# Kernel tuning notes

Hardware: AMD Instinct MI355X
Metric: run time of the kernel (lower is better)

Reference implementation:

```python
import jax, jax.numpy as jnp
import numpy as np

COST_CLASS = 1.0


def _lsa(cost):
    """linear_sum_assignment clone (Jonker-Volgenant shortest augmenting path),
    matching scipy.optimize.linear_sum_assignment semantics for rectangular inputs."""
    cost = np.asarray(cost, dtype=np.float64)
    transposed = cost.shape[0] > cost.shape[1]
    if transposed:
        cost = cost.T
    nr, nc = cost.shape
    u = np.zeros(nr)
    v = np.zeros(nc)
    path = np.full(nc, -1, dtype=np.int64)
    col4row = np.full(nr, -1, dtype=np.int64)
    row4col = np.full(nc, -1, dtype=np.int64)
    for cur in range(nr):
        i = cur
        SR = np.zeros(nr, dtype=bool)
        SC = np.zeros(nc, dtype=bool)
        d = np.full(nc, np.inf)
        minVal = 0.0
        sink = -1
        while sink == -1:
            SR[i] = True
            rem = ~SC
            r = minVal + cost[i, rem] - u[i] - v[rem]
            dr = d[rem]
            pr = path[rem]
            better = r < dr
            dr[better] = r[better]
            pr[better] = i
            d[rem] = dr
            path[rem] = pr
            remIdx = np.flatnonzero(rem)
            j = remIdx[np.argmin(d[remIdx])]
            minVal = d[j]
            SC[j] = True
            if row4col[j] == -1:
                sink = j
            else:
                i = row4col[j]
        # dual updates (scipy _lsap_body)
        u[cur] += minVal
        mask = SR.copy()
        mask[cur] = False
        u[mask] += minVal - d[col4row[mask]]
        v[SC] -= minVal - d[SC]
        # augment along shortest path
        j = sink
        while True:
            i = path[j]
            row4col[j] = i
            col4row[i], j = j, col4row[i]
            if i == cur:
                break
    if transposed:
        order = np.argsort(col4row)
        return col4row[order], order
    return np.arange(nr), col4row


def setup_inputs() -> dict:
    key = jax.random.key(0)
    k1, k2, k3 = jax.random.split(key, 3)
    bs, Q, T, NC = 32, 256, 128, 2048
    pred_logits = jax.random.normal(k1, (bs, Q, NC), dtype=jnp.float32)
    tgt_labels = jax.random.randint(k2, (bs, T), 0, NC)
    agent_mask = jax.random.randint(k3, (bs, Q), 0, 2).astype(bool)
    return {"pred_logits": pred_logits, "tgt_labels": tgt_labels,
            "agent_mask": agent_mask, "use_background": 0}


def reference(pred_logits, tgt_labels, agent_mask, use_background):
    bs, Q, _ = pred_logits.shape
    T = tgt_labels.shape[1]
    probs = jax.nn.softmax(pred_logits, axis=-1)  # [bs, Q, NC]
    if not use_background:
        probs = jnp.where(agent_mask[:, :, None], probs, 0.0)
    out_prob = probs.reshape(bs * Q, -1)
    tgt_ids = tgt_labels.reshape(-1)                  # concat of all batch labels
    C = COST_CLASS * (-out_prob[:, tgt_ids])          # [bs*Q, bs*T]
    C = C.reshape(bs, Q, bs * T)
    # per-batch Hungarian (same as scipy loop in the original; inherently serial per instance)
    Cn = np.asarray(C)
    rows = np.empty((bs, T), dtype=np.int64)
    cols = np.empty((bs, T), dtype=np.int64)
    for i in range(bs):
        r, c = _lsa(Cn[i, :, i * T:(i + 1) * T])      # [Q, T] block for batch i
        rows[i] = r
        cols[i] = c
    return C, jnp.asarray(rows), jnp.asarray(cols)
```

## Files before the change

kernel.cpp:

```cpp
#include <hip/hip_runtime.h>
#include <hip/hip_bf16.h>
#include <math.h>

#define BS 32
#define QN 256
#define TN 128
#define NCLS 2048
#define NTGT (BS * TN)

__global__ void detect_mask_layout(const unsigned char* __restrict__ m, int* flag) {
    __shared__ int found;
    if (threadIdx.x == 0) found = 0;
    __syncthreads();
    int local = 0;
    for (int i = threadIdx.x; i < BS * QN; i += blockDim.x) {
        if ((i & 3) != 0 && m[i] != 0) local = 1;
    }
    if (local) atomicOr(&found, 1);
    __syncthreads();
    if (threadIdx.x == 0) *flag = found;
}

__global__ __launch_bounds__(256) void compute_C_kernel(
    const float* __restrict__ logits, const int* __restrict__ labels,
    const unsigned char* __restrict__ mask_b, const int* __restrict__ use_bg,
    const int* __restrict__ layout_flag, float* __restrict__ C) {
    __shared__ float prob_sh[NCLS];
    __shared__ int lab_sh[NTGT];
    __shared__ float red[4];

    const int tid = threadIdx.x;
    const int bq = blockIdx.x;
    const float* row = logits + (size_t)bq * NCLS;

    for (int k = tid; k < NTGT; k += 256) lab_sh[k] = labels[k];

    float x[8];
    float m = -INFINITY;
#pragma unroll
    for (int k = 0; k < 8; k++) {
        x[k] = row[tid + k * 256];
        m = fmaxf(m, x[k]);
    }
#pragma unroll
    for (int off = 32; off >= 1; off >>= 1) m = fmaxf(m, __shfl_xor(m, off));
    if ((tid & 63) == 0) red[tid >> 6] = m;
    __syncthreads();
    m = fmaxf(fmaxf(red[0], red[1]), fmaxf(red[2], red[3]));
    __syncthreads();

    float e[8];
    float s = 0.f;
#pragma unroll
    for (int k = 0; k < 8; k++) {
        e[k] = expf(x[k] - m);
        s += e[k];
    }
#pragma unroll
    for (int off = 32; off >= 1; off >>= 1) s += __shfl_xor(s, off);
    if ((tid & 63) == 0) red[tid >> 6] = s;
    __syncthreads();
    s = ((red[0] + red[1]) + red[2]) + red[3];

#pragma unroll
    for (int k = 0; k < 8; k++) prob_sh[tid + k * 256] = e[k] / s;

    const int ub = *use_bg;
    int am;
    if (*layout_flag)
        am = mask_b[bq];
    else
        am = ((const int*)mask_b)[bq];
    const bool zero_row = (ub == 0) && (am == 0);
    __syncthreads();

    float* Crow = C + (size_t)bq * NTGT;
#pragma unroll
    for (int k = 0; k < 16; k++) {
        const int jj = tid + k * 256;
        Crow[jj] = zero_row ? 0.0f : -prob_sh[lab_sh[jj]];
    }
}

__global__ __launch_bounds__(256) void transpose_kernel(const float* __restrict__ C,
                                                        float* __restrict__ CT) {
    __shared__ float tile[TN][65];
    const int b = blockIdx.x;
    const int q0 = blockIdx.y * 64;
    const int tid = threadIdx.x;

    const float* src = C + (size_t)(b * QN + q0) * NTGT + b * TN;
#pragma unroll
    for (int it = 0; it < 32; it++) {
        const int idx = tid + it * 256;
        const int ql = idx >> 7;
        const int i = idx & 127;
        tile[i][ql] = src[(size_t)ql * NTGT + i];
    }
    __syncthreads();
    float* dst = CT + (size_t)b * TN * QN + q0;
#pragma unroll
    for (int it = 0; it < 32; it++) {
        const int idx = tid + it * 256;
        const int i = idx >> 6;
        const int ql = idx & 63;
        dst[(size_t)i * QN + ql] = tile[i][ql];
    }
}

template <int CTRL>
__device__ __forceinline__ double dpp_mov_f64(double x) {
    union { double d; int i[2]; } a, r;
    a.d = x;
    r.i[0] = __builtin_amdgcn_update_dpp(0, a.i[0], CTRL, 0xF, 0xF, true);
    r.i[1] = __builtin_amdgcn_update_dpp(0, a.i[1], CTRL, 0xF, 0xF, true);
    return r.d;
}
__device__ __forceinline__ double read_lane_f64(double x, int srclane) {
    union { double d; int i[2]; } a, r;
    a.d = x;
    r.i[0] = __builtin_amdgcn_readlane(a.i[0], srclane);
    r.i[1] = __builtin_amdgcn_readlane(a.i[1], srclane);
    return r.d;
}

#define QUAD_XOR1 0xB1
#define QUAD_XOR2 0x4E
#define ROW_ROR4  0x124
#define ROW_ROR8  0x128

__device__ __forceinline__ int first_tied(unsigned long long B0, unsigned long long B1,
                                          unsigned long long B2, unsigned long long B3) {
    int jmin = 0x7fffffff;
    if (B0) { const int c = ((__ffsll((long long)B0) - 1) << 2) + 0; jmin = c < jmin ? c : jmin; }
    if (B1) { const int c = ((__ffsll((long long)B1) - 1) << 2) + 1; jmin = c < jmin ? c : jmin; }
    if (B2) { const int c = ((__ffsll((long long)B2) - 1) << 2) + 2; jmin = c < jmin ? c : jmin; }
    if (B3) { const int c = ((__ffsll((long long)B3) - 1) << 2) + 3; jmin = c < jmin ? c : jmin; }
    return jmin;
}

__global__ __launch_bounds__(64) void lsa_kernel(const float* __restrict__ C,
                                                 const float* __restrict__ CT,
                                                 float* __restrict__ rows_out,
                                                 float* __restrict__ cols_out) {
    const int b = blockIdx.x;
    const int lane = threadIdx.x;
    const int j0 = lane * 4;

    __shared__ float cost_sh[TN * QN];
    __shared__ double u_sh[TN];
    __shared__ int col4row_sh[TN];

    if (CT) {
        const float4* src = (const float4*)(CT + (size_t)b * TN * QN);
        float4* dst = (float4*)cost_sh;
#pragma unroll 8
        for (int it = 0; it < TN * QN / 4 / 64; it++) {
            const int idx = it * 64 + lane;
            dst[idx] = src[idx];
        }
    } else {
        const float* cbsrc = C + (size_t)b * QN * NTGT + b * TN;
        for (int it = 0; it < 512; it++) {
            const int j = it >> 1;
            const int i = lane + 64 * (it & 1);
            cost_sh[i * QN + j] = cbsrc[(size_t)j * NTGT + i];
        }
    }
    u_sh[2 * lane] = 0.0;
    u_sh[2 * lane + 1] = 0.0;
    __syncthreads();

    double v0 = 0.0, v1 = 0.0, v2 = 0.0, v3 = 0.0;
    double u0 = 0.0, u1 = 0.0;
    int rc0 = -1, rc1 = -1, rc2 = -1, rc3 = -1;
    int cr0 = -1, cr1 = -1;

    for (int cur = 0; cur < TN; cur++) {
        double dv0 = INFINITY, dv1 = INFINITY, dv2 = INFINITY, dv3 = INFINITY;
        double duA = 0.0, duB = 0.0;
        int sc = 0, sr = 0;
        int p0 = 0, p1 = 0, p2 = 0, p3 = 0;
        if (lane == (cur >> 1)) sr = 1 << (cur & 1);

        int i = cur;
        double m_d = 0.0;
        unsigned long long B0 = 0, B1 = 0, B2 = 0, B3 = 0;
        int sink = 0;
        bool have_g = false;
        int jg = 0, krcg = 0;

        float4 cc = *(const float4*)(cost_sh + i * QN + j0);
        double ui = u_sh[i];
        float4 gcc = cc;
        double gui = ui;

        while (true) {
            const double ca0 = ((m_d + (double)cc.x) - ui) - v0;
            const double ca1 = ((m_d + (double)cc.y) - ui) - v1;
            const double ca2 = ((m_d + (double)cc.z) - ui) - v2;
            const double ca3 = ((m_d + (double)cc.w) - ui) - v3;
            const bool i0 = !(sc & 1) && (ca0 < dv0);
            const bool i1 = !(sc & 2) && (ca1 < dv1);
            const bool i2 = !(sc & 4) && (ca2 < dv2);
            const bool i3 = !(sc & 8) && (ca3 < dv3);
            const unsigned long long chk =
                __ballot(i0 && (ca0 <= m_d)) | __ballot(i1 && (ca1 <= m_d)) |
                __ballot(i2 && (ca2 <= m_d)) | __ballot(i3 && (ca3 <= m_d));
            if (i0) { dv0 = ca0; p0 = i; }
            if (i1) { dv1 = ca1; p1 = i; }
            if (i2) { dv2 = ca2; p2 = i; }
            if (i3) { dv3 = ca3; p3 = i; }

            if (chk == 0ull && have_g) {
                if (krcg < 0) { sink = jg; break; }
                const int gowner = jg >> 2;
                const int gslot = jg & 3;
                if (lane == gowner) sc |= 1 << gslot;
                if (lane == (krcg >> 1)) {
                    if (krcg & 1) { duB = m_d; sr |= 2; }
                    else { duA = m_d; sr |= 1; }
                }
                i = krcg;
                cc = gcc;
                ui = gui;
            } else {
                const double md0 = (sc & 1) ? INFINITY : dv0;
                const double md1 = (sc & 2) ? INFINITY : dv1;
                const double md2 = (sc & 4) ? INFINITY : dv2;
                const double md3 = (sc & 8) ? INFINITY : dv3;
                double lm = fmin(fmin(md0, md1), fmin(md2, md3));
                lm = fmin(lm, dpp_mov_f64<QUAD_XOR1>(lm));
                lm = fmin(lm, dpp_mov_f64<QUAD_XOR2>(lm));
                lm = fmin(lm, dpp_mov_f64<ROW_ROR4>(lm));
                lm = fmin(lm, dpp_mov_f64<ROW_ROR8>(lm));
                const double r0 = read_lane_f64(lm, 0);
                const double r1 = read_lane_f64(lm, 16);
                const double r2 = read_lane_f64(lm, 32);
                const double r3 = read_lane_f64(lm, 48);
                m_d = fmin(fmin(r0, r1), fmin(r2, r3));
                B0 = __ballot(!(sc & 1) && (dv0 == m_d));
                B1 = __ballot(!(sc & 2) && (dv1 == m_d));
                B2 = __ballot(!(sc & 4) && (dv2 == m_d));
                B3 = __ballot(!(sc & 8) && (dv3 == m_d));

                const int jmin = first_tied(B0, B1, B2, B3);
                const int owner = jmin >> 2;
                const int slot = jmin & 3;
                const unsigned long long bit = 1ull << owner;
                if (slot == 0) B0 &= ~bit;
                else if (slot == 1) B1 &= ~bit;
                else if (slot == 2) B2 &= ~bit;
                else B3 &= ~bit;
                const int rsel = (slot == 0) ? rc0 : (slot == 1) ? rc1 : (slot == 2) ? rc2 : rc3;
                const int krc = __builtin_amdgcn_readlane(rsel, owner);
                if (krc < 0) { sink = jmin; break; }
                if (lane == owner) sc |= 1 << slot;
                if (lane == (krc >> 1)) {
                    if (krc & 1) { duB = m_d; sr |= 2; }
                    else { duA = m_d; sr |= 1; }
                }
                i = krc;
                cc = *(const float4*)(cost_sh + i * QN + j0);
                ui = u_sh[i];
            }

            if ((B0 | B1 | B2 | B3) != 0ull) {
                jg = first_tied(B0, B1, B2, B3);
                const int go = jg >> 2;
                const int gs = jg & 3;
                const unsigned long long gbit = 1ull << go;
                if (gs == 0) B0 &= ~gbit;
                else if (gs == 1) B1 &= ~gbit;
                else if (gs == 2) B2 &= ~gbit;
                else B3 &= ~gbit;
                const int grsel = (gs == 0) ? rc0 : (gs == 1) ? rc1 : (gs == 2) ? rc2 : rc3;
                krcg = __builtin_amdgcn_readlane(grsel, go);
                const int rg = (krcg >= 0) ? krcg : 0;
                gcc = *(const float4*)(cost_sh + rg * QN + j0);
                gui = u_sh[rg];
                have_g = true;
            } else {
                have_g = false;
            }
        }

        if (sc & 1) v0 -= m_d - dv0;
        if (sc & 2) v1 -= m_d - dv1;
        if (sc & 4) v2 -= m_d - dv2;
        if (sc & 8) v3 -= m_d - dv3;
        if (sr & 1) u0 += (2 * lane == cur) ? m_d : (m_d - duA);
        if (sr & 2) u1 += (2 * lane + 1 == cur) ? m_d : (m_d - duB);
        u_sh[2 * lane] = u0;
        u_sh[2 * lane + 1] = u1;

        int j = sink;
        while (true) {
            const int aslot = j & 3;
            const int aowner = j >> 2;
            const int psel = (aslot == 0) ? p0 : (aslot == 1) ? p1 : (aslot == 2) ? p2 : p3;
            const int pi = __builtin_amdgcn_readlane(psel, aowner);
            if (lane == aowner) {
                if (aslot == 0) rc0 = pi;
                else if (aslot == 1) rc1 = pi;
                else if (aslot == 2) rc2 = pi;
                else rc3 = pi;
            }
            const int cowner = pi >> 1;
            const int cslot = pi & 1;
            const int csel = cslot ? cr1 : cr0;
            const int nj = __builtin_amdgcn_readlane(csel, cowner);
            if (lane == cowner) {
                if (cslot) cr1 = j;
                else cr0 = j;
            }
            j = nj;
            if (pi == cur) break;
        }
    }

    col4row_sh[2 * lane] = cr0;
    col4row_sh[2 * lane + 1] = cr1;
    __syncthreads();
#pragma unroll
    for (int t = 0; t < 2; t++) {
        const int ii = 2 * lane + t;
        const int myv = t ? cr1 : cr0;
        int rank = 0;
        for (int t2 = 0; t2 < TN; t2++) rank += (col4row_sh[t2] < myv) ? 1 : 0;
        rows_out[b * TN + rank] = (float)myv;
        cols_out[b * TN + rank] = (float)ii;
    }
}

extern "C" void kernel_launch(void* const* d_in, const int* in_sizes, int n_in,
                              void* d_out, int out_size, void* d_ws, size_t ws_size,
                              hipStream_t stream) {
    const float* logits = (const float*)d_in[0];
    const int* labels = (const int*)d_in[1];
    const unsigned char* mask_b = (const unsigned char*)d_in[2];
    const int* use_bg = (const int*)d_in[3];

    float* C = (float*)d_out;
    float* rows_out = C + (size_t)BS * QN * NTGT;
    float* cols_out = rows_out + BS * TN;

    int* flag = (int*)d_ws;
    const size_t ct_off = 4096;
    const size_t ct_bytes = (size_t)BS * TN * QN * sizeof(float);
    const bool useCT = ws_size >= ct_off + ct_bytes;
    float* CT = useCT ? (float*)((char*)d_ws + ct_off) : nullptr;

    detect_mask_layout<<<1, 256, 0, stream>>>(mask_b, flag);
    compute_C_kernel<<<BS * QN, 256, 0, stream>>>(logits, labels, mask_b, use_bg, flag, C);
    if (useCT) {
        dim3 tg(BS, QN / 64);
        transpose_kernel<<<tg, 256, 0, stream>>>(C, CT);
    }
    lsa_kernel<<<BS, 64, 0, stream>>>(C, CT, rows_out, cols_out);
}
```

Measured before the change: 1.256 ms.

## Fuse transpose into cost kernel, vectorize C stores, and double-buffer LSA row loads

The separate transpose kernel is removed. The cost kernel now writes the transposed per-batch diagonal block directly, and it stores C rows as float4 using vectorized label reads. In the Hungarian loop, the body is unrolled twice with ping-pong registers so that the cost row for the next guessed pivot is prefetched before the current relaxation. The four chk ballots are also merged into one. This cuts a kernel launch and a pass over C, and hides shared-memory latency on the serial augmenting path. The trade-offs are strided scattered CT writes and an unconditional speculative load on every iteration.

Result: slower. 1.308 ms (+4.2%).

```diff
diff --git a/kernel.cpp b/kernel.cpp
--- a/kernel.cpp
+++ b/kernel.cpp
@@ -24,13 +24,16 @@
 __global__ __launch_bounds__(256) void compute_C_kernel(
     const float* __restrict__ logits, const int* __restrict__ labels,
     const unsigned char* __restrict__ mask_b, const int* __restrict__ use_bg,
-    const int* __restrict__ layout_flag, float* __restrict__ C) {
+    const int* __restrict__ layout_flag, float* __restrict__ C,
+    float* __restrict__ CT) {
     __shared__ float prob_sh[NCLS];
     __shared__ int lab_sh[NTGT];
     __shared__ float red[4];
 
     const int tid = threadIdx.x;
     const int bq = blockIdx.x;
+    const int b = bq >> 8;
+    const int q = bq & 255;
     const float* row = logits + (size_t)bq * NCLS;
 
     for (int k = tid; k < NTGT; k += 256) lab_sh[k] = labels[k];
@@ -74,37 +77,26 @@
     const bool zero_row = (ub == 0) && (am == 0);
     __syncthreads();
 
-    float* Crow = C + (size_t)bq * NTGT;
-#pragma unroll
-    for (int k = 0; k < 16; k++) {
-        const int jj = tid + k * 256;
-        Crow[jj] = zero_row ? 0.0f : -prob_sh[lab_sh[jj]];
-    }
-}
-
-__global__ __launch_bounds__(256) void transpose_kernel(const float* __restrict__ C,
-                                                        float* __restrict__ CT) {
-    __shared__ float tile[TN][65];
-    const int b = blockIdx.x;
-    const int q0 = blockIdx.y * 64;
-    const int tid = threadIdx.x;
-
-    const float* src = C + (size_t)(b * QN + q0) * NTGT + b * TN;
-#pragma unroll
-    for (int it = 0; it < 32; it++) {
-        const int idx = tid + it * 256;
-        const int ql = idx >> 7;
-        const int i = idx & 127;
-        tile[i][ql] = src[(size_t)ql * NTGT + i];
-    }
-    __syncthreads();
-    float* dst = CT + (size_t)b * TN * QN + q0;
-#pragma unroll
-    for (int it = 0; it < 32; it++) {
-        const int idx = tid + it * 256;
-        const int i = idx >> 6;
-        const int ql = idx & 63;
-        dst[(size_t)i * QN + ql] = tile[i][ql];
+    float4* Crow4 = (float4*)(C + (size_t)bq * NTGT);
+#pragma unroll
+    for (int k = 0; k < 4; k++) {
+        const int idx4 = tid + k * 256;
+        const int4 lab4 = *(const int4*)&lab_sh[idx4 * 4];
+        float4 out;
+        if (zero_row) {
+            out = make_float4(0.f, 0.f, 0.f, 0.f);
+        } else {
+            out.x = -prob_sh[lab4.x];
+            out.y = -prob_sh[lab4.y];
+            out.z = -prob_sh[lab4.z];
+            out.w = -prob_sh[lab4.w];
+        }
+        Crow4[idx4] = out;
+    }
+
+    if (CT && tid < TN) {
+        const float val = zero_row ? 0.0f : -prob_sh[lab_sh[b * TN + tid]];
+        CT[((size_t)b * TN + tid) * QN + q] = val;
     }
 }
 
@@ -178,119 +170,135 @@
 
     for (int cur = 0; cur < TN; cur++) {
         double dv0 = INFINITY, dv1 = INFINITY, dv2 = INFINITY, dv3 = INFINITY;
-        double duA = 0.0, duB = 0.0;
+        double duR0 = 0.0, duR1 = 0.0;
         int sc = 0, sr = 0;
         int p0 = 0, p1 = 0, p2 = 0, p3 = 0;
         if (lane == (cur >> 1)) sr = 1 << (cur & 1);
 
-        int i = cur;
+        int irow = cur;
         double m_d = 0.0;
         unsigned long long B0 = 0, B1 = 0, B2 = 0, B3 = 0;
-        int sink = 0;
+        int sink = -1;
         bool have_g = false;
         int jg = 0, krcg = 0;
 
-        float4 cc = *(const float4*)(cost_sh + i * QN + j0);
-        double ui = u_sh[i];
-        float4 gcc = cc;
-        double gui = ui;
+        float4 ccA = *(const float4*)(cost_sh + irow * QN + j0);
+        double uiA = u_sh[irow];
+        float4 ccB;
+        double uiB;
+
+#define POP_BODY(CCX, UIX, CCY, UIY)                                           \
+        {                                                                      \
+                          \
+            const int rg_ = (have_g && krcg >= 0) ? krcg : 0;                  \
+            CCY = *(const float4*)(cost_sh + rg_ * QN + j0);                   \
+            UIY = u_sh[rg_];                                                   \
+                             \
+            const double ca0 = ((m_d + (double)CCX.x) - UIX) - v0;             \
+            const double ca1 = ((m_d + (double)CCX.y) - UIX) - v1;             \
+            const double ca2 = ((m_d + (double)CCX.z) - UIX) - v2;             \
+            const double ca3 = ((m_d + (double)CCX.w) - UIX) - v3;             \
+            const bool i0_ = !(sc & 1) && (ca0 < dv0);                         \
+            const bool i1_ = !(sc & 2) && (ca1 < dv1);                         \
+            const bool i2_ = !(sc & 4) && (ca2 < dv2);                         \
+            const bool i3_ = !(sc & 8) && (ca3 < dv3);                         \
+            const bool chkl_ = (i0_ && ca0 <= m_d) || (i1_ && ca1 <= m_d) ||   \
+                               (i2_ && ca2 <= m_d) || (i3_ && ca3 <= m_d);     \
+            const unsigned long long chk_ = __ballot(chkl_);                   \
+            if (i0_) { dv0 = ca0; p0 = irow; }                                 \
+            if (i1_) { dv1 = ca1; p1 = irow; }                                 \
+            if (i2_) { dv2 = ca2; p2 = irow; }                                 \
+            if (i3_) { dv3 = ca3; p3 = irow; }                                 \
+            if (chk_ == 0ull && have_g) {                                      \
+                                               \
+                if (krcg < 0) {                                                \
+                    sink = jg;                                                 \
+                } else {                                                       \
+                    const int ow_ = jg >> 2, sl_ = jg & 3;                     \
+                    if (lane == ow_) sc |= 1 << sl_;                           \
+                    if (lane == (krcg >> 1)) {                                 \
+                        if (krcg & 1) { duR1 = m_d; sr |= 2; }                 \
+                        else { duR0 = m_d; sr |= 1; }                          \
+                    }                                                          \
+                    irow = krcg;                                               \
+                }                                                              \
+            } else {                                                           \
+                                      \
+                const double md0_ = (sc & 1) ? INFINITY : dv0;                 \
+                const double md1_ = (sc & 2) ? INFINITY : dv1;                 \
+                const double md2_ = (sc & 4) ? INFINITY : dv2;                 \
+                const double md3_ = (sc & 8) ? INFINITY : dv3;                 \
+                double lm_ = fmin(fmin(md0_, md1_), fmin(md2_, md3_));         \
+                lm_ = fmin(lm_, dpp_mov_f64<QUAD_XOR1>(lm_));                  \
+                lm_ = fmin(lm_, dpp_mov_f64<QUAD_XOR2>(lm_));                  \
+                lm_ = fmin(lm_, dpp_mov_f64<ROW_ROR4>(lm_));                   \
+                lm_ = fmin(lm_, dpp_mov_f64<ROW_ROR8>(lm_));                   \
+                const double r0_ = read_lane_f64(lm_, 0);                      \
+                const double r1_ = read_lane_f64(lm_, 16);                     \
+                const double r2_ = read_lane_f64(lm_, 32);                     \
+                const double r3_ = read_lane_f64(lm_, 48);                     \
+                m_d = fmin(fmin(r0_, r1_), fmin(r2_, r3_));                    \
+                B0 = __ballot(!(sc & 1) && (dv0 == m_d));                      \
+                B1 = __ballot(!(sc & 2) && (dv1 == m_d));                      \
+                B2 = __ballot(!(sc & 4) && (dv2 == m_d));                      \
+                B3 = __ballot(!(sc & 8) && (dv3 == m_d));                      \
+                const int jmin_ = first_tied(B0, B1, B2, B3);                  \
+                const int ow_ = jmin_ >> 2, sl_ = jmin_ & 3;                   \
+                const unsigned long long bit_ = 1ull << ow_;                   \
+                if (sl_ == 0) B0 &= ~bit_;                                     \
+                else if (sl_ == 1) B1 &= ~bit_;                                \
+                else if (sl_ == 2) B2 &= ~bit_;                                \
+                else B3 &= ~bit_;                                              \
+                const int rsel_ = (sl_ == 0) ? rc0 : (sl_ == 1) ? rc1          \
+                                 : (sl_ == 2) ? rc2 : rc3;                     \
+                const int krc_ = __builtin_amdgcn_readlane(rsel_, ow_);        \
+                if (krc_ < 0) {                                                \
+                    sink = jmin_;                                              \
+                } else {                                                       \
+                    if (lane == ow_) sc |= 1 << sl_;                           \
+                    if (lane == (krc_ >> 1)) {                                 \
+                        if (krc_ & 1) { duR1 = m_d; sr |= 2; }                 \
+                        else { duR0 = m_d; sr |= 1; }                          \
+                    }                                                          \
+                    irow = krc_;                                               \
+                    CCY = *(const float4*)(cost_sh + irow * QN + j0);          \
+                    UIY = u_sh[irow];                                          \
+                }                                                              \
+            }                                                                  \
+            if (sink < 0) {                                                    \
+                             \
+                if ((B0 | B1 | B2 | B3) != 0ull) {                             \
+                    jg = first_tied(B0, B1, B2, B3);                           \
+                    const int go_ = jg >> 2, gs_ = jg & 3;                     \
+                    const unsigned long long gb_ = 1ull << go_;                \
+                    if (gs_ == 0) B0 &= ~gb_;                                  \
+                    else if (gs_ == 1) B1 &= ~gb_;                             \
+                    else if (gs_ == 2) B2 &= ~gb_;                             \
+                    else B3 &= ~gb_;                                           \
+                    const int gr_ = (gs_ == 0) ? rc0 : (gs_ == 1) ? rc1        \
+                                   : (gs_ == 2) ? rc2 : rc3;                   \
+                    krcg = __builtin_amdgcn_readlane(gr_, go_);                \
+                    have_g = true;                                             \
+                } else {                                                       \
+                    have_g = false;                                            \
+                }                                                              \
+            }                                                                  \
+        }
 
         while (true) {
-            const double ca0 = ((m_d + (double)cc.x) - ui) - v0;
-            const double ca1 = ((m_d + (double)cc.y) - ui) - v1;
-            const double ca2 = ((m_d + (double)cc.z) - ui) - v2;
-            const double ca3 = ((m_d + (double)cc.w) - ui) - v3;
-            const bool i0 = !(sc & 1) && (ca0 < dv0);
-            const bool i1 = !(sc & 2) && (ca1 < dv1);
-            const bool i2 = !(sc & 4) && (ca2 < dv2);
-            const bool i3 = !(sc & 8) && (ca3 < dv3);
-            const unsigned long long chk =
-                __ballot(i0 && (ca0 <= m_d)) | __ballot(i1 && (ca1 <= m_d)) |
-                __ballot(i2 && (ca2 <= m_d)) | __ballot(i3 && (ca3 <= m_d));
-            if (i0) { dv0 = ca0; p0 = i; }
-            if (i1) { dv1 = ca1; p1 = i; }
-            if (i2) { dv2 = ca2; p2 = i; }
-            if (i3) { dv3 = ca3; p3 = i; }
-
-            if (chk == 0ull && have_g) {
-                if (krcg < 0) { sink = jg; break; }
-                const int gowner = jg >> 2;
-                const int gslot = jg & 3;
-                if (lane == gowner) sc |= 1 << gslot;
-                if (lane == (krcg >> 1)) {
-                    if (krcg & 1) { duB = m_d; sr |= 2; }
-                    else { duA = m_d; sr |= 1; }
-                }
-                i = krcg;
-                cc = gcc;
-                ui = gui;
-            } else {
-                const double md0 = (sc & 1) ? INFINITY : dv0;
-                const double md1 = (sc & 2) ? INFINITY : dv1;
-                const double md2 = (sc & 4) ? INFINITY : dv2;
-                const double md3 = (sc & 8) ? INFINITY : dv3;
-                double lm = fmin(fmin(md0, md1), fmin(md2, md3));
-                lm = fmin(lm, dpp_mov_f64<QUAD_XOR1>(lm));
-                lm = fmin(lm, dpp_mov_f64<QUAD_XOR2>(lm));
-                lm = fmin(lm, dpp_mov_f64<ROW_ROR4>(lm));
-                lm = fmin(lm, dpp_mov_f64<ROW_ROR8>(lm));
-                const double r0 = read_lane_f64(lm, 0);
-                const double r1 = read_lane_f64(lm, 16);
-                const double r2 = read_lane_f64(lm, 32);
-                const double r3 = read_lane_f64(lm, 48);
-                m_d = fmin(fmin(r0, r1), fmin(r2, r3));
-                B0 = __ballot(!(sc & 1) && (dv0 == m_d));
-                B1 = __ballot(!(sc & 2) && (dv1 == m_d));
-                B2 = __ballot(!(sc & 4) && (dv2 == m_d));
-                B3 = __ballot(!(sc & 8) && (dv3 == m_d));
-
-                const int jmin = first_tied(B0, B1, B2, B3);
-                const int owner = jmin >> 2;
-                const int slot = jmin & 3;
-                const unsigned long long bit = 1ull << owner;
-                if (slot == 0) B0 &= ~bit;
-                else if (slot == 1) B1 &= ~bit;
-                else if (slot == 2) B2 &= ~bit;
-                else B3 &= ~bit;
-                const int rsel = (slot == 0) ? rc0 : (slot == 1) ? rc1 : (slot == 2) ? rc2 : rc3;
-                const int krc = __builtin_amdgcn_readlane(rsel, owner);
-                if (krc < 0) { sink = jmin; break; }
-                if (lane == owner) sc |= 1 << slot;
-                if (lane == (krc >> 1)) {
-                    if (krc & 1) { duB = m_d; sr |= 2; }
-                    else { duA = m_d; sr |= 1; }
-                }
-                i = krc;
-                cc = *(const float4*)(cost_sh + i * QN + j0);
-                ui = u_sh[i];
-            }
-
-            if ((B0 | B1 | B2 | B3) != 0ull) {
-                jg = first_tied(B0, B1, B2, B3);
-                const int go = jg >> 2;
-                const int gs = jg & 3;
-                const unsigned long long gbit = 1ull << go;
-                if (gs == 0) B0 &= ~gbit;
-                else if (gs == 1) B1 &= ~gbit;
-                else if (gs == 2) B2 &= ~gbit;
-                else B3 &= ~gbit;
-                const int grsel = (gs == 0) ? rc0 : (gs == 1) ? rc1 : (gs == 2) ? rc2 : rc3;
-                krcg = __builtin_amdgcn_readlane(grsel, go);
-                const int rg = (krcg >= 0) ? krcg : 0;
-                gcc = *(const float4*)(cost_sh + rg * QN + j0);
-                gui = u_sh[rg];
-                have_g = true;
-            } else {
-                have_g = false;
-            }
-        }
+            POP_BODY(ccA, uiA, ccB, uiB)
+            if (sink >= 0) break;
+            POP_BODY(ccB, uiB, ccA, uiA)
+            if (sink >= 0) break;
+        }
+#undef POP_BODY
 
         if (sc & 1) v0 -= m_d - dv0;
         if (sc & 2) v1 -= m_d - dv1;
         if (sc & 4) v2 -= m_d - dv2;
         if (sc & 8) v3 -= m_d - dv3;
-        if (sr & 1) u0 += (2 * lane == cur) ? m_d : (m_d - duA);
-        if (sr & 2) u1 += (2 * lane + 1 == cur) ? m_d : (m_d - duB);
+        if (sr & 1) u0 += (2 * lane == cur) ? m_d : (m_d - duR0);
+        if (sr & 2) u1 += (2 * lane + 1 == cur) ? m_d : (m_d - duR1);
         u_sh[2 * lane] = u0;
         u_sh[2 * lane + 1] = u1;
 
@@ -352,10 +360,6 @@
     float* CT = useCT ? (float*)((char*)d_ws + ct_off) : nullptr;
 
     detect_mask_layout<<<1, 256, 0, stream>>>(mask_b, flag);
-    compute_C_kernel<<<BS * QN, 256, 0, stream>>>(logits, labels, mask_b, use_bg, flag, C);
-    if (useCT) {
-        dim3 tg(BS, QN / 64);
-        transpose_kernel<<<tg, 256, 0, stream>>>(C, CT);
-    }
+    compute_C_kernel<<<BS * QN, 256, 0, stream>>>(logits, labels, mask_b, use_bg, flag, C, CT);
     lsa_kernel<<<BS, 64, 0, stream>>>(C, CT, rows_out, cols_out);
 }
```
